# Kernel optimization log

Measured on AMD Instinct MI355X. Metric: run time of the kernel, lower is better.

## Reference

```python
import jax, jax.numpy as jnp
import numpy as np

B, S, CL = 64, 250, 16
WV, CV, FV, LAB = 50000, 100, 10, 20
WD, CD, CH, FD, HD = 300, 300, 50, 5, 200
T = LAB + 2          # CRF lattice size (labels + START + STOP)
START, STOP = LAB, LAB + 1
H = HD // 2          # hidden per LSTM direction
IN = CH + WD + FD    # 355


def _lstm_dir(x, m, w_ih, w_hh, b):
    # x: [B,S,IN], m: [B,S] bool -> masked unidirectional LSTM (PyTorch gate order i,f,g,o)
    Bn = x.shape[0]
    def step(carry, inp):
        h, c = carry
        xt, mt = inp
        g = xt @ w_ih.T + h @ w_hh.T + b
        i, f, gg, o = jnp.split(g, 4, axis=-1)
        c_new = jax.nn.sigmoid(f) * c + jax.nn.sigmoid(i) * jnp.tanh(gg)
        h_new = jax.nn.sigmoid(o) * jnp.tanh(c_new)
        mt = mt[:, None]
        h = jnp.where(mt, h_new, h)
        c = jnp.where(mt, c_new, c)
        return (h, c), h
    init = (jnp.zeros((Bn, H), x.dtype), jnp.zeros((Bn, H), x.dtype))
    _, hs = jax.lax.scan(step, init, (x.transpose(1, 0, 2), m.T))
    return hs.transpose(1, 0, 2)  # [B,S,H]


def _viterbi(feats, mask, trans):
    # feats: [B,S,T], mask: [B,S] bool, trans: [T,T] (trans[i,j] = score i->j)
    Bn = feats.shape[0]
    delta0 = trans[START][None, :] + feats[:, 0]  # [B,T]
    ident = jnp.arange(T)[None, :]
    def step(delta, inp):
        f_t, m_t = inp                              # [B,T], [B]
        sc = delta[:, :, None] + trans[None]        # [B,T(prev),T(cur)]
        vmax = sc.max(axis=1)
        bp = sc.argmax(axis=1)                      # [B,T]
        m = m_t[:, None]
        delta = jnp.where(m, vmax + f_t, delta)
        bp = jnp.where(m, bp, ident)                # pads: pass-through pointer
        return delta, bp
    delta, bps = jax.lax.scan(step, delta0,
                              (feats[:, 1:].transpose(1, 0, 2), mask[:, 1:].T))
    final = delta + trans[:, STOP][None, :]
    score = final.max(axis=1)                       # [B]
    last = final.argmax(axis=1)                     # [B]
    ar = jnp.arange(Bn)
    def back(tag, bp):
        prev = bp[ar, tag]
        return prev, prev
    _, prevs = jax.lax.scan(back, last, bps, reverse=True)  # [S-1,B]
    tag_seq = jnp.concatenate([prevs.transpose(1, 0), last[:, None]], axis=1)  # [B,S]
    return score, tag_seq


def setup_inputs() -> dict:
    key = jax.random.key(0)
    ks = jax.random.split(key, 20)
    lens = jax.random.randint(ks[0], (B,), S // 2, S + 1)
    mask = (jnp.arange(S)[None, :] < lens[:, None])
    def u(k, shape, scale):
        return jax.random.uniform(k, shape, jnp.float32, -scale, scale)
    return {
        "batch_word": jax.random.randint(ks[1], (B, S), 0, WV),
        "batch_features": jax.random.randint(ks[2], (B, S), 0, FV),
        "batch_wordlen": lens,
        "batch_char": jax.random.randint(ks[3], (B * S, CL), 0, CV),
        "batch_charlen": jax.random.randint(ks[4], (B * S,), 1, CL + 1),
        "batch_charrecover": jnp.arange(B * S),
        "mask": mask,
        "char_emb": u(ks[5], (CV, CD), np.sqrt(3.0 / CD)),
        "word_emb": u(ks[6], (WV, WD), np.sqrt(3.0 / WD)),
        "feat_emb": u(ks[7], (FV, FD), np.sqrt(3.0 / FD)),
        "conv_w": 0.1 * jax.random.normal(ks[8], (CH, CD, 3), jnp.float32),
        "conv_b": jnp.zeros((CH,), jnp.float32),
        "w_ih_f": 0.1 * jax.random.normal(ks[9], (4 * H, IN), jnp.float32),
        "w_hh_f": 0.1 * jax.random.normal(ks[10], (4 * H, H), jnp.float32),
        "b_f": jnp.zeros((4 * H,), jnp.float32),
        "w_ih_b": 0.1 * jax.random.normal(ks[11], (4 * H, IN), jnp.float32),
        "w_hh_b": 0.1 * jax.random.normal(ks[12], (4 * H, H), jnp.float32),
        "b_b": jnp.zeros((4 * H,), jnp.float32),
        "proj_w": 0.1 * jax.random.normal(ks[13], (HD, T), jnp.float32),
        "proj_b": jnp.zeros((T,), jnp.float32),
        "trans": 0.1 * jax.random.normal(ks[14], (T, T), jnp.float32),
    }


def reference(batch_word, batch_features, batch_wordlen, batch_char, batch_charlen,
              batch_charrecover, mask, char_emb, word_emb, feat_emb, conv_w, conv_b,
              w_ih_f, w_hh_f, b_f, w_ih_b, w_hh_b, b_b, proj_w, proj_b, trans):
    # char CNN: embed -> conv1d(k=3, pad=1) -> global max-pool (dropout: eval mode, identity)
    ce = char_emb[batch_char]                          # [B*S, CL, CD]
    conv = jax.lax.conv_general_dilated(
        ce.transpose(0, 2, 1), conv_w, window_strides=(1,), padding=[(1, 1)],
        dimension_numbers=('NCH', 'OIH', 'NCH')) + conv_b[None, :, None]
    char_feat = conv.max(axis=2)                       # [B*S, CH]
    char_feat = char_feat[batch_charrecover].reshape(B, S, CH)
    word_rep = jnp.concatenate(
        [word_emb[batch_word], char_feat, feat_emb[batch_features]], axis=2)  # [B,S,IN]
    # masked BiLSTM (equivalent to pack_padded_sequence: pads never update state)
    h_f = _lstm_dir(word_rep, mask, w_ih_f, w_hh_f, b_f)
    h_b = _lstm_dir(word_rep[:, ::-1], mask[:, ::-1], w_ih_b, w_hh_b, b_b)[:, ::-1]
    lstm_out = jnp.concatenate([h_f, h_b], axis=2)     # [B,S,HD]
    feats = lstm_out @ proj_w + proj_b                 # [B,S,T]
    score, tag_seq = _viterbi(feats, mask, trans)
    return tag_seq
```

## Files before the change

### kernel.cpp

```cpp
#include <hip/hip_runtime.h>
#include <hip/hip_bf16.h>
#include <math.h>

#define WS_U        0
#define WS_WPAD     15360
#define WS_WREP     359424
#define WS_PRE      6503424
#define WS_LSTM     359424
#define WS_FEATS    3559424

__global__ __launch_bounds__(256) void prepw_kernel(
    const float* __restrict__ wf, const float* __restrict__ wb,
    float* __restrict__ w_pad) {
  int idx = blockIdx.x * 256 + threadIdx.x;
  if (idx >= 896 * 384) return;
  int col = idx % 384, row = idx / 384;
  float v = 0.f;
  if (col < 355) {
    if (row < 400)      v = wf[row * 355 + col];
    else if (row < 800) v = wb[(row - 400) * 355 + col];
  }
  w_pad[idx] = v;
}

__global__ __launch_bounds__(256) void u_kernel(
    const float* __restrict__ char_emb, const float* __restrict__ conv_w,
    float* __restrict__ U) {
  int idx = blockIdx.x * 256 + threadIdx.x;
  if (idx >= 15000) return;
  int c = idx / 150, rem = idx % 150, k = rem / 50, o = rem % 50;
  float acc = 0.f;
  for (int i = 0; i < 300; i++)
    acc += char_emb[c * 300 + i] * conv_w[(o * 300 + i) * 3 + k];
  U[idx] = acc;
}

__global__ __launch_bounds__(64) void assemble_kernel(
    const int* __restrict__ batch_word, const int* __restrict__ batch_feats,
    const int* __restrict__ batch_char, const int* __restrict__ recover,
    const float* __restrict__ word_emb, const float* __restrict__ feat_emb,
    const float* __restrict__ conv_b, const float* __restrict__ U,
    float* __restrict__ wrep) {
  int n = blockIdx.x;
  int tid = threadIdx.x;
  __shared__ int ch[16];
  if (tid < 16) ch[tid] = batch_char[(size_t)recover[n] * 16 + tid];
  __syncthreads();
  float* dst = wrep + (size_t)n * 384;
  int w = batch_word[n];
  for (int i = tid; i < 300; i += 64) dst[i] = word_emb[(size_t)w * 300 + i];
  if (tid < 34) {
    int i = 350 + tid;
    dst[i] = (i < 355) ? feat_emb[batch_feats[n] * 5 + (i - 350)] : 0.f;
  }
  if (tid < 50) {
    int o = tid;
    float bo = conv_b[o];
    float m = -1e30f;
#pragma unroll
    for (int l = 0; l < 16; l++) {
      float v = bo + U[(ch[l] * 3 + 1) * 50 + o];
      if (l > 0)  v += U[(ch[l - 1] * 3 + 0) * 50 + o];
      if (l < 15) v += U[(ch[l + 1] * 3 + 2) * 50 + o];
      m = fmaxf(m, v);
    }
    dst[300 + o] = m;
  }
}

__global__ __launch_bounds__(256, 4) void gemm_kernel(
    const float* __restrict__ A, const float* __restrict__ B,
    float* __restrict__ C, const float* __restrict__ bf,
    const float* __restrict__ bb) {
  __shared__ float As[16][128];
  __shared__ float Bs[16][128];
  int tid = threadIdx.x;
  int m0 = blockIdx.x * 128;
  int n0 = blockIdx.y * 128;
  int tx = tid & 15, ty = tid >> 4;
  int lr = tid >> 2;
  int lc = (tid & 3) * 4;
  float acc[8][8];
#pragma unroll
  for (int i = 0; i < 8; i++)
#pragma unroll
    for (int j = 0; j < 8; j++) acc[i][j] = 0.f;

  for (int k0 = 0; k0 < 384; k0 += 16) {
#pragma unroll
    for (int h = 0; h < 2; h++) {
      int row = lr + h * 64;
      float4 av = *(const float4*)(A + (size_t)(m0 + row) * 384 + k0 + lc);
      As[lc + 0][row] = av.x; As[lc + 1][row] = av.y;
      As[lc + 2][row] = av.z; As[lc + 3][row] = av.w;
      float4 bv = *(const float4*)(B + (size_t)(n0 + row) * 384 + k0 + lc);
      Bs[lc + 0][row] = bv.x; Bs[lc + 1][row] = bv.y;
      Bs[lc + 2][row] = bv.z; Bs[lc + 3][row] = bv.w;
    }
    __syncthreads();
#pragma unroll
    for (int k = 0; k < 16; k++) {
      float a[8], b[8];
      *(float4*)&a[0] = *(const float4*)&As[k][ty * 8];
      *(float4*)&a[4] = *(const float4*)&As[k][ty * 8 + 4];
      *(float4*)&b[0] = *(const float4*)&Bs[k][tx * 8];
      *(float4*)&b[4] = *(const float4*)&Bs[k][tx * 8 + 4];
#pragma unroll
      for (int i = 0; i < 8; i++)
#pragma unroll
        for (int j = 0; j < 8; j++) acc[i][j] += a[i] * b[j];
    }
    __syncthreads();
  }
#pragma unroll
  for (int i = 0; i < 8; i++) {
    int m = m0 + ty * 8 + i;
#pragma unroll
    for (int jj = 0; jj < 8; jj++) {
      int j = n0 + tx * 8 + jj;
      if (j < 800) {
        float bias = (j < 400) ? bf[j] : bb[j - 400];
        C[(size_t)m * 800 + j] = acc[i][jj] + bias;
      }
    }
  }
}

__global__ __launch_bounds__(256, 2) void lstm_kernel(
    const float* __restrict__ pre, const float* __restrict__ w_hh_f,
    const float* __restrict__ w_hh_b, const int* __restrict__ wordlen,
    float* __restrict__ lstm_out) {
  int tid = threadIdx.x;
  int dir = blockIdx.x >> 6;
  int r = blockIdx.x & 63;
  int len = wordlen[r];
  const float* __restrict__ Wh = dir ? w_hh_b : w_hh_f;
  __shared__ float h_sh[128];
  __shared__ float g_sh[400];
  float W1[100], W2[100];
  int j1 = tid, j2 = tid + 200;
  if (tid < 200) {
    const float4* w1 = (const float4*)(Wh + j1 * 100);
    const float4* w2 = (const float4*)(Wh + j2 * 100);
#pragma unroll
    for (int q = 0; q < 25; q++) {
      float4 a = w1[q], b = w2[q];
      W1[4 * q] = a.x; W1[4 * q + 1] = a.y; W1[4 * q + 2] = a.z; W1[4 * q + 3] = a.w;
      W2[4 * q] = b.x; W2[4 * q + 1] = b.y; W2[4 * q + 2] = b.z; W2[4 * q + 3] = b.w;
    }
  }
  if (tid < 128) h_sh[tid] = 0.f;
  float c_reg = 0.f;
  const float* __restrict__ pr = pre + dir * 400;
  int p0 = dir ? 249 : 0;
  int dp = dir ? -1 : 1;
  size_t rowbase = (size_t)r * 250;
  float pv1 = 0.f, pv2 = 0.f;
  if (tid < 200) {
    size_t off = (rowbase + p0) * 800;
    pv1 = pr[off + j1];
    pv2 = pr[off + j2];
  }
  __syncthreads();
  for (int i = 0; i < 250; i++) {
    int p = p0 + dp * i;
    if (tid < 200) {
      float g1 = pv1, g2 = pv2;
      if (i < 249) {
        size_t off = (rowbase + p + dp) * 800;
        pv1 = pr[off + j1];
        pv2 = pr[off + j2];
      }
#pragma unroll
      for (int q = 0; q < 25; q++) {
        float4 hv = *(const float4*)&h_sh[4 * q];
        g1 += hv.x * W1[4 * q]     + hv.y * W1[4 * q + 1]
            + hv.z * W1[4 * q + 2] + hv.w * W1[4 * q + 3];
        g2 += hv.x * W2[4 * q]     + hv.y * W2[4 * q + 1]
            + hv.z * W2[4 * q + 2] + hv.w * W2[4 * q + 3];
      }
      g_sh[j1] = g1;
      g_sh[j2] = g2;
    }
    __syncthreads();
    if (tid < 100) {
      float gi = g_sh[tid], gf = g_sh[100 + tid];
      float gg = g_sh[200 + tid], go = g_sh[300 + tid];
      float hv;
      if (p < len) {
        float si = 1.f / (1.f + expf(-gi));
        float sf = 1.f / (1.f + expf(-gf));
        float so = 1.f / (1.f + expf(-go));
        c_reg = sf * c_reg + si * tanhf(gg);
        hv = so * tanhf(c_reg);
        h_sh[tid] = hv;
      } else {
        hv = h_sh[tid];
      }
      lstm_out[(rowbase + p) * 200 + dir * 100 + tid] = hv;
    }
    __syncthreads();
  }
}

__global__ __launch_bounds__(256) void proj_kernel(
    const float* __restrict__ lstm_out, const float* __restrict__ proj_w,
    const float* __restrict__ proj_b, float* __restrict__ feats) {
  __shared__ float L[8][200];
  int tid = threadIdx.x;
  size_t base = (size_t)blockIdx.x * 8 * 200;
  for (int idx = tid; idx < 1600; idx += 256)
    L[idx / 200][idx % 200] = lstm_out[base + idx];
  __syncthreads();
  int ty = tid >> 5, c = tid & 31;
  if (c < 22) {
    float acc = proj_b[c];
#pragma unroll 8
    for (int k = 0; k < 200; k++) acc += L[ty][k] * proj_w[k * 22 + c];
    feats[((size_t)blockIdx.x * 8 + ty) * 22 + c] = acc;
  }
}

__global__ __launch_bounds__(64) void viterbi_kernel(
    const float* __restrict__ feats, const float* __restrict__ trans,
    const int* __restrict__ wordlen, int* __restrict__ out) {
  int r = blockIdx.x;
  int lane = threadIdx.x;
  __shared__ float dsh[22];
  __shared__ float tsh[22][23];
  __shared__ unsigned char bps[250][22];
  int len = wordlen[r];
  const float* __restrict__ fr = feats + (size_t)r * 250 * 22;
  for (int idx = lane; idx < 484; idx += 64)
    tsh[idx / 22][idx % 22] = trans[idx];
  if (lane < 22) dsh[lane] = trans[20 * 22 + lane] + fr[lane];
  __syncthreads();
  for (int t = 1; t < 250; t++) {
    float best = -1e30f, fv = 0.f;
    int arg = 0;
    if (lane < 22) {
      fv = fr[t * 22 + lane];
#pragma unroll
      for (int k = 0; k < 22; k++) {
        float cand = dsh[k] + tsh[k][lane];
        if (cand > best) { best = cand; arg = k; }
      }
    }
    __syncthreads();
    if (lane < 22) {
      bool valid = t < len;
      if (valid) dsh[lane] = best + fv;
      bps[t][lane] = valid ? (unsigned char)arg : (unsigned char)lane;
    }
    __syncthreads();
  }
  if (lane == 0) {
    float best = -1e30f;
    int last = 0;
#pragma unroll
    for (int k = 0; k < 22; k++) {
      float cand = dsh[k] + tsh[k][21];
      if (cand > best) { best = cand; last = k; }
    }
    int tag = last;
    out[r * 250 + 249] = tag;
    for (int t = 249; t >= 1; t--) {
      tag = bps[t][tag];
      out[r * 250 + t - 1] = tag;
    }
  }
}

extern "C" void kernel_launch(void* const* d_in, const int* in_sizes, int n_in,
                              void* d_out, int out_size, void* d_ws, size_t ws_size,
                              hipStream_t stream) {
  const int* batch_word  = (const int*)d_in[0];
  const int* batch_feats = (const int*)d_in[1];
  const int* wordlen     = (const int*)d_in[2];
  const int* batch_char  = (const int*)d_in[3];
  const int* recover     = (const int*)d_in[5];
  const float* char_emb  = (const float*)d_in[7];
  const float* word_emb  = (const float*)d_in[8];
  const float* feat_emb  = (const float*)d_in[9];
  const float* conv_w    = (const float*)d_in[10];
  const float* conv_b    = (const float*)d_in[11];
  const float* w_ih_f    = (const float*)d_in[12];
  const float* w_hh_f    = (const float*)d_in[13];
  const float* b_f       = (const float*)d_in[14];
  const float* w_ih_b    = (const float*)d_in[15];
  const float* w_hh_b    = (const float*)d_in[16];
  const float* b_b       = (const float*)d_in[17];
  const float* proj_w    = (const float*)d_in[18];
  const float* proj_b    = (const float*)d_in[19];
  const float* trans     = (const float*)d_in[20];
  int* out = (int*)d_out;
  float* ws = (float*)d_ws;

  float* U        = ws + WS_U;
  float* w_pad    = ws + WS_WPAD;
  float* wrep     = ws + WS_WREP;
  float* pre      = ws + WS_PRE;
  float* lstm_out = ws + WS_LSTM;
  float* feats    = ws + WS_FEATS;

  prepw_kernel<<<1344, 256, 0, stream>>>(w_ih_f, w_ih_b, w_pad);
  u_kernel<<<59, 256, 0, stream>>>(char_emb, conv_w, U);
  assemble_kernel<<<16000, 64, 0, stream>>>(batch_word, batch_feats, batch_char,
                                            recover, word_emb, feat_emb, conv_b,
                                            U, wrep);
  dim3 ggrid(125, 7);
  gemm_kernel<<<ggrid, 256, 0, stream>>>(wrep, w_pad, pre, b_f, b_b);
  lstm_kernel<<<128, 256, 0, stream>>>(pre, w_hh_f, w_hh_b, wordlen, lstm_out);
  proj_kernel<<<2000, 256, 0, stream>>>(lstm_out, proj_w, proj_b, feats);
  viterbi_kernel<<<64, 64, 0, stream>>>(feats, trans, wordlen, out);
}
```

Baseline: 795.4 us.

## Restructure LSTM recurrence with paired-lane gate exchange and double-buffered hidden state

```diff
diff --git a/kernel.cpp b/kernel.cpp
--- a/kernel.cpp
+++ b/kernel.cpp
@@ -126,81 +126,97 @@
   }
 }
 
-__global__ __launch_bounds__(256, 2) void lstm_kernel(
+__global__ __launch_bounds__(256, 1) void lstm_kernel(
     const float* __restrict__ pre, const float* __restrict__ w_hh_f,
     const float* __restrict__ w_hh_b, const int* __restrict__ wordlen,
     float* __restrict__ lstm_out) {
-  int tid = threadIdx.x;
+  int t = threadIdx.x;
   int dir = blockIdx.x >> 6;
   int r = blockIdx.x & 63;
   int len = wordlen[r];
   const float* __restrict__ Wh = dir ? w_hh_b : w_hh_f;
-  __shared__ float h_sh[128];
-  __shared__ float g_sh[400];
-  float W1[100], W2[100];
-  int j1 = tid, j2 = tid + 200;
-  if (tid < 200) {
-    const float4* w1 = (const float4*)(Wh + j1 * 100);
-    const float4* w2 = (const float4*)(Wh + j2 * 100);
-#pragma unroll
-    for (int q = 0; q < 25; q++) {
-      float4 a = w1[q], b = w2[q];
-      W1[4 * q] = a.x; W1[4 * q + 1] = a.y; W1[4 * q + 2] = a.z; W1[4 * q + 3] = a.w;
-      W2[4 * q] = b.x; W2[4 * q + 1] = b.y; W2[4 * q + 2] = b.z; W2[4 * q + 3] = b.w;
-    }
-  }
-  if (tid < 128) h_sh[tid] = 0.f;
-  float c_reg = 0.f;
+  __shared__ __align__(16) float h0[112];
+  __shared__ __align__(16) float h1[112];
+
+  const int j = t >> 1;
+  const int odd = t & 1;
+  const int rA = odd * 100 + j;
+  const int rB = rA + 200;
+  float4 WA[25], WB[25];
+  if (t < 200) {
+    const float4* wa = (const float4*)(Wh + (size_t)rA * 100);
+    const float4* wb = (const float4*)(Wh + (size_t)rB * 100);
+#pragma unroll
+    for (int q = 0; q < 25; q++) { WA[q] = wa[q]; WB[q] = wb[q]; }
+  }
+  if (t < 112) { h0[t] = 0.f; h1[t] = 0.f; }
+
+  float c_reg = 0.f, h_reg = 0.f;
   const float* __restrict__ pr = pre + dir * 400;
-  int p0 = dir ? 249 : 0;
-  int dp = dir ? -1 : 1;
-  size_t rowbase = (size_t)r * 250;
-  float pv1 = 0.f, pv2 = 0.f;
-  if (tid < 200) {
-    size_t off = (rowbase + p0) * 800;
-    pv1 = pr[off + j1];
-    pv2 = pr[off + j2];
+  const int p0 = dir ? 249 : 0;
+  const int dp = dir ? -1 : 1;
+  const size_t rowbase = (size_t)r * 250;
+  const int j1 = rA;
+  const int j2 = rB;
+
+  float pvA1 = 0.f, pvA2 = 0.f, pvB1 = 0.f, pvB2 = 0.f;
+  if (t < 200) {
+    size_t offA = (rowbase + (size_t)p0) * 800;
+    pvA1 = pr[offA + j1]; pvA2 = pr[offA + j2];
+    size_t offB = (rowbase + (size_t)(p0 + dp)) * 800;
+    pvB1 = pr[offB + j1]; pvB2 = pr[offB + j2];
   }
   __syncthreads();
-  for (int i = 0; i < 250; i++) {
-    int p = p0 + dp * i;
-    if (tid < 200) {
-      float g1 = pv1, g2 = pv2;
-      if (i < 249) {
-        size_t off = (rowbase + p + dp) * 800;
-        pv1 = pr[off + j1];
-        pv2 = pr[off + j2];
-      }
-#pragma unroll
-      for (int q = 0; q < 25; q++) {
-        float4 hv = *(const float4*)&h_sh[4 * q];
-        g1 += hv.x * W1[4 * q]     + hv.y * W1[4 * q + 1]
-            + hv.z * W1[4 * q + 2] + hv.w * W1[4 * q + 3];
-        g2 += hv.x * W2[4 * q]     + hv.y * W2[4 * q + 1]
-            + hv.z * W2[4 * q + 2] + hv.w * W2[4 * q + 3];
-      }
-      g_sh[j1] = g1;
-      g_sh[j2] = g2;
-    }
-    __syncthreads();
-    if (tid < 100) {
-      float gi = g_sh[tid], gf = g_sh[100 + tid];
-      float gg = g_sh[200 + tid], go = g_sh[300 + tid];
-      float hv;
-      if (p < len) {
-        float si = 1.f / (1.f + expf(-gi));
-        float sf = 1.f / (1.f + expf(-gf));
-        float so = 1.f / (1.f + expf(-go));
-        c_reg = sf * c_reg + si * tanhf(gg);
-        hv = so * tanhf(c_reg);
-        h_sh[tid] = hv;
-      } else {
-        hv = h_sh[tid];
-      }
-      lstm_out[(rowbase + p) * 200 + dir * 100 + tid] = hv;
-    }
-    __syncthreads();
-  }
+
+#define LSTM_STEP(I, HRD, HWR, V1, V2)                                         \
+  do {                                                                         \
+    const int p = p0 + dp * (I);                                               \
+    const bool valid = (p < len);                    \
+    float g1 = 0.f, g2 = 0.f;                                                  \
+    if (valid && t < 200) {                                                    \
+      g1 = V1; g2 = V2;                                                        \
+      _Pragma("unroll")                                                        \
+      for (int q = 0; q < 25; q++) {                                           \
+        float4 hv = *(const float4*)&(HRD)[4 * q];                             \
+        g1 += hv.x * WA[q].x + hv.y * WA[q].y + hv.z * WA[q].z +               \
+              hv.w * WA[q].w;                                                  \
+        g2 += hv.x * WB[q].x + hv.y * WB[q].y + hv.z * WB[q].z +               \
+              hv.w * WB[q].w;                                                  \
+      }                                                                        \
+    }                                                                          \
+    if (t < 200) {              \
+      const int ip = ((I) + 2 < 250) ? (I) + 2 : (I);                          \
+      const size_t offp = (rowbase + (size_t)(p0 + dp * ip)) * 800;            \
+      V1 = pr[offp + j1];                                                      \
+      V2 = pr[offp + j2];                                                      \
+    }                                                                          \
+    if (valid) {                                                               \
+      const float gi_in = __shfl_xor(g1, 1, 64);   \
+      const float gg_in = __shfl_xor(g2, 1, 64);   \
+      if (t < 200 && odd) {                                                    \
+        const float si = 1.f / (1.f + expf(-gi_in));                           \
+        const float sf = 1.f / (1.f + expf(-g1));                              \
+        const float so = 1.f / (1.f + expf(-g2));                              \
+        c_reg = sf * c_reg + si * tanhf(gg_in);                                \
+        h_reg = so * tanhf(c_reg);                                             \
+        (HWR)[j] = h_reg;                                                      \
+        lstm_out[(rowbase + (size_t)p) * 200 + dir * 100 + j] = h_reg;         \
+      }                                                                        \
+         \
+      asm volatile("s_waitcnt lgkmcnt(0)" ::: "memory");                       \
+      __builtin_amdgcn_s_barrier();                                           \
+    } else if (t < 200 && odd) {                                               \
+                  \
+      lstm_out[(rowbase + (size_t)p) * 200 + dir * 100 + j] = h_reg;           \
+    }                                                                          \
+  } while (0)
+
+#pragma unroll 1
+  for (int ii = 0; ii < 250; ii += 2) {
+    LSTM_STEP(ii,     h0, h1, pvA1, pvA2);
+    LSTM_STEP(ii + 1, h1, h0, pvB1, pvB2);
+  }
+#undef LSTM_STEP
 }
 
 __global__ __launch_bounds__(256) void proj_kernel(
```

Result: no change. 809.7 us (+1.8%).
